# Performance work log

Measured on AMD Instinct MI355X. Metric: run time of the kernel, lower is better.

Reference implementation:

```python
import jax, jax.numpy as jnp
import numpy as np

# Problem dims
N_LIG, N_PROT = 10000, 40000
N = N_LIG + N_PROT            # total nodes in batched graph
E = 400000                    # total edges (avg degree 8)
B = 512                       # number of pocket graphs in batch
F_LIG, F_PROT = 74, 1280      # ligand / protein node feature dims
H, D = 4, 64                  # GAT heads, per-head dim
HD = H * D                    # hidden size == PROJ_DIM == 256


def setup_inputs() -> dict:
    key = jax.random.key(0)
    ks = jax.random.split(key, 16)
    s = jnp.float32(0.05)  # keep activations tame
    return {
        "ligand_x":  jax.random.normal(ks[0], (N_LIG, F_LIG), jnp.float32),
        "protein_x": jax.random.normal(ks[1], (N_PROT, F_PROT), jnp.float32),
        "W_lig":  jax.random.normal(ks[2], (F_LIG, HD), jnp.float32) * s,
        "W_prot": jax.random.normal(ks[3], (F_PROT, HD), jnp.float32) * s,
        "W1":     jax.random.normal(ks[4], (HD, HD), jnp.float32) * s,
        "a1_src": jax.random.normal(ks[5], (H, D), jnp.float32) * s,
        "a1_dst": jax.random.normal(ks[6], (H, D), jnp.float32) * s,
        "W2":     jax.random.normal(ks[7], (HD, HD), jnp.float32) * s,
        "a2_src": jax.random.normal(ks[8], (H, D), jnp.float32) * s,
        "a2_dst": jax.random.normal(ks[9], (H, D), jnp.float32) * s,
        "W_out":  jax.random.normal(ks[10], (HD + 1, 1), jnp.float32) * s,
        "b_out":  jnp.zeros((1,), jnp.float32),
        "edge_src":  jax.random.randint(ks[11], (E,), 0, N, jnp.int32),
        "edge_dst":  jax.random.randint(ks[12], (E,), 0, N, jnp.int32),
        "graph_ids": jnp.sort(jax.random.randint(ks[13], (N,), 0, B, jnp.int32)),
        "scores":    jax.random.uniform(ks[14], (B, 1), jnp.float32),
    }


def _gat_layer(x, W, a_src, a_dst, src, dst):
    """Multi-head GAT layer over an edge list. x:[N,HD] -> [N,HD]."""
    n = x.shape[0]
    h = (x @ W).reshape(n, H, D)                               # [N,H,D]
    att_s = jnp.einsum('nhd,hd->nh', h, a_src)                 # [N,H]
    att_d = jnp.einsum('nhd,hd->nh', h, a_dst)
    e = jax.nn.leaky_relu(att_s[src] + att_d[dst], 0.2)        # [E,H]
    # edge softmax over incoming edges of each destination node
    m = jax.ops.segment_max(e, dst, num_segments=n)            # [N,H]
    w = jnp.exp(e - m[dst])                                    # [E,H]
    denom = jax.ops.segment_sum(w, dst, num_segments=n)        # [N,H]
    agg = jax.ops.segment_sum(h[src] * w[..., None], dst, num_segments=n)  # [N,H,D]
    out = agg / (denom[..., None] + 1e-9)
    return jax.nn.elu(out).reshape(n, HD)


def reference(ligand_x, protein_x, W_lig, W_prot, W1, a1_src, a1_dst,
              W2, a2_src, a2_dst, W_out, b_out,
              edge_src, edge_dst, graph_ids, scores):
    # per-node-type input projection into shared hidden space
    x = jnp.concatenate([ligand_x @ W_lig, protein_x @ W_prot], axis=0)  # [N,HD]
    h = _gat_layer(x, W1, a1_src, a1_dst, edge_src, edge_dst)
    h = _gat_layer(h, W2, a2_src, a2_dst, edge_src, edge_dst)
    # mean pooling per graph -> [B, PROJ_DIM]
    gsum = jax.ops.segment_sum(h, graph_ids, num_segments=B)
    cnt = jax.ops.segment_sum(jnp.ones((h.shape[0], 1), h.dtype), graph_ids, num_segments=B)
    pooled = gsum / jnp.maximum(cnt, 1.0)
    # concat docking score, final linear (dropout is identity at eval)
    feat = jnp.concatenate([pooled, scores], axis=1)           # [B, PROJ_DIM+1]
    return feat @ W_out + b_out                                 # [B,1]
```

## Files before the change

kernel.cpp:

```cpp
#include <hip/hip_runtime.h>
#include <hip/hip_bf16.h>

#define N_LIG   10000
#define N_PROT  40000
#define NN      50000
#define EDGES   400000
#define BATCH   512
#define F_LIG   74
#define F_PROT  1280
#define HD      256
#define HEADS   4
#define DIM     64

typedef __bf16 bf16x8 __attribute__((ext_vector_type(8)));
typedef __bf16 bf16x4 __attribute__((ext_vector_type(4)));
typedef float  f32x4  __attribute__((ext_vector_type(4)));


__global__ void k_hist(const int* __restrict__ dst, int* __restrict__ counts, int E) {
    int e = blockIdx.x * blockDim.x + threadIdx.x;
    if (e < E) atomicAdd(&counts[dst[e]], 1);
}

__global__ __launch_bounds__(1024) void k_scan1(const int* __restrict__ counts,
                                                int* __restrict__ incl,
                                                int* __restrict__ bsum, int N) {
    __shared__ int tmp[1024];
    int i = blockIdx.x * 1024 + threadIdx.x;
    int v = (i < N) ? counts[i] : 0;
    tmp[threadIdx.x] = v;
    __syncthreads();
    for (int off = 1; off < 1024; off <<= 1) {
        int add = (threadIdx.x >= (unsigned)off) ? tmp[threadIdx.x - off] : 0;
        __syncthreads();
        tmp[threadIdx.x] += add;
        __syncthreads();
    }
    if (i < N) incl[i] = tmp[threadIdx.x];
    if (threadIdx.x == 1023) bsum[blockIdx.x] = tmp[1023];
}

__global__ void k_scan2(int* __restrict__ bsum, int nb, int* __restrict__ row_ptr, int N, int E) {
    if (threadIdx.x == 0 && blockIdx.x == 0) {
        int run = 0;
        for (int i = 0; i < nb; ++i) { int v = bsum[i]; bsum[i] = run; run += v; }
        row_ptr[N] = E;
    }
}

__global__ __launch_bounds__(1024) void k_scan3(const int* __restrict__ incl,
                                                const int* __restrict__ counts,
                                                const int* __restrict__ bsum,
                                                int* __restrict__ row_ptr, int N) {
    int i = blockIdx.x * 1024 + threadIdx.x;
    if (i < N) row_ptr[i] = bsum[blockIdx.x] + incl[i] - counts[i];
}

__global__ void k_scatter(const int* __restrict__ src, const int* __restrict__ dst,
                          const int* __restrict__ row_ptr, int* __restrict__ cursor,
                          int* __restrict__ csr_src, int E) {
    int e = blockIdx.x * blockDim.x + threadIdx.x;
    if (e < E) {
        int d = dst[e];
        int pos = row_ptr[d] + atomicAdd(&cursor[d], 1);
        csr_src[pos] = src[e];
    }
}

__global__ __launch_bounds__(256) void k_wcvt(const float* __restrict__ W,
                                              __bf16* __restrict__ Bt, int K, int Kp) {
    int n = blockIdx.x;
    for (int k = threadIdx.x; k < Kp; k += blockDim.x)
        Bt[(size_t)n * Kp + k] = (k < K) ? (__bf16)W[(size_t)k * HD + n] : (__bf16)0.f;
}

__global__ __launch_bounds__(128) void k_apad(const float* __restrict__ A, float* __restrict__ Ap) {
    int row = blockIdx.x, t = threadIdx.x;
    if (t < 96) Ap[(size_t)row * 96 + t] = (t < F_LIG) ? A[(size_t)row * F_LIG + t] : 0.f;
}

__device__ __forceinline__ void gload16(const void* g, void* l) {
    __builtin_amdgcn_global_load_lds(
        (const __attribute__((address_space(1))) void*)g,
        (__attribute__((address_space(3))) void*)l, 16, 0, 0);
}

__device__ __forceinline__ int xcd_swz(int orig, int nwg) {
    int q = nwg >> 3, r = nwg & 7;
    int xcd = orig & 7, idx = orig >> 3;
    return (xcd < r ? xcd * (q + 1) : r * (q + 1) + (xcd - r) * q) + idx;
}

template <int MODE>
__global__ __launch_bounds__(256, 3)
void mfma_gemm(const float* __restrict__ A, const __bf16* __restrict__ Bt,
               float* __restrict__ C,
               __bf16* __restrict__ Hbf, float* __restrict__ atts, float* __restrict__ attd,
               const float* __restrict__ a_src, const float* __restrict__ a_dst,
               int M, int K, int Kp, int nwg) {
    __shared__ __align__(16) unsigned char smem[49152];
    float*  sA = (float*)smem;
    __bf16* sB = (__bf16*)(smem + 24576);

    int wg   = xcd_swz(blockIdx.x, nwg);
    int tid  = threadIdx.x;
    int bm   = (wg >> 1) * 64;
    int bn   = (wg & 1) * 128;
    int lane = tid & 63, wave = tid >> 6;
    int wr   = wave >> 1, wc = wave & 1;
    int l15  = lane & 15, quad = lane >> 4;

    f32x4 acc[2][4];
    #pragma unroll
    for (int i = 0; i < 2; ++i)
        #pragma unroll
        for (int j = 0; j < 4; ++j)
            acc[i][j] = (f32x4){0.f, 0.f, 0.f, 0.f};

    int caA = wave * 2;
    int rlA = lane >> 3, csA = (lane & 7) ^ rlA;
    int rlB = lane >> 2, csB = (lane & 3) ^ (rlB & 3);

    int gmA[2];
    const __bf16* gB[2];
    #pragma unroll
    for (int it = 0; it < 2; ++it) {
        int gm = bm + (caA + it) * 8 + rlA;
        gmA[it] = (gm < M) ? gm : (M - 1);
        gB[it] = Bt + (size_t)(bn + (caA + it) * 16 + rlB) * Kp + csB * 8;
    }

    auto stage = [&](int buf, int k0) {
        #pragma unroll
        for (int it = 0; it < 2; ++it)
            gload16(A + (size_t)gmA[it] * K + k0 + csA * 4,
                    sA + buf * 2048 + (caA + it) * 256);
        #pragma unroll
        for (int it = 0; it < 2; ++it)
            gload16(gB[it] + k0,
                    sB + buf * 4096 + (caA + it) * 512);
    };

    int nsteps = K >> 5;

    stage(0, 0);
    if (nsteps > 1) {
        stage(1, 32);
        asm volatile("s_waitcnt vmcnt(4)" ::: "memory");
    } else {
        asm volatile("s_waitcnt vmcnt(0)" ::: "memory");
    }
    __builtin_amdgcn_s_barrier();
    __builtin_amdgcn_sched_barrier(0);

    int cur = 0, stg = 2;
    for (int s = 0; s < nsteps; ++s) {
        if (s + 2 < nsteps) stage(stg, (s + 2) * 32);

        bf16x8 bfr[4];
        #pragma unroll
        for (int j = 0; j < 4; ++j) {
            int rowb = wc * 64 + j * 16 + l15;
            int ch = quad ^ (l15 & 3);
            bfr[j] = *(const bf16x8*)&sB[cur * 4096 + rowb * 32 + ch * 8];
        }
        bf16x8 af[2], al[2];
        #pragma unroll
        for (int i = 0; i < 2; ++i) {
            int rowa = wr * 32 + i * 16 + l15;
            int ch0 = (quad * 2)     ^ (l15 & 7);
            int ch1 = (quad * 2 + 1) ^ (l15 & 7);
            f32x4 p0 = *(const f32x4*)&sA[cur * 2048 + rowa * 32 + ch0 * 4];
            f32x4 p1 = *(const f32x4*)&sA[cur * 2048 + rowa * 32 + ch1 * 4];
            #pragma unroll
            for (int c = 0; c < 8; ++c) {
                float x = (c < 4) ? p0[c] : p1[c - 4];
                __bf16 h = (__bf16)x;
                af[i][c] = h;
                if (MODE) al[i][c] = (__bf16)(x - (float)h);
            }
        }

        #pragma unroll
        for (int i = 0; i < 2; ++i)
            #pragma unroll
            for (int j = 0; j < 4; ++j) {
                acc[i][j] = __builtin_amdgcn_mfma_f32_16x16x32_bf16(af[i], bfr[j], acc[i][j], 0, 0, 0);
                if (MODE)
                    acc[i][j] = __builtin_amdgcn_mfma_f32_16x16x32_bf16(al[i], bfr[j], acc[i][j], 0, 0, 0);
            }

        asm volatile("s_waitcnt lgkmcnt(0)" ::: "memory");
        __builtin_amdgcn_sched_barrier(0);
        if (s + 2 < nsteps)      asm volatile("s_waitcnt vmcnt(4)" ::: "memory");
        else if (s + 1 < nsteps) asm volatile("s_waitcnt vmcnt(0)" ::: "memory");
        __builtin_amdgcn_s_barrier();
        __builtin_amdgcn_sched_barrier(0);

        cur = (cur == 2) ? 0 : cur + 1;
        stg = (stg == 2) ? 0 : stg + 1;
    }

    if (MODE == 0) {
        #pragma unroll
        for (int i = 0; i < 2; ++i)
            #pragma unroll
            for (int r = 0; r < 4; ++r) {
                int m = bm + wr * 32 + i * 16 + quad * 4 + r;
                if (m < M) {
                    #pragma unroll
                    for (int j = 0; j < 4; ++j)
                        C[(size_t)m * HD + bn + wc * 64 + j * 16 + l15] = acc[i][j][r];
                }
            }
    } else {
        int head = (bn >> 6) + wc;
        float as[4], ad2[4];
        #pragma unroll
        for (int j = 0; j < 4; ++j) {
            as[j]  = a_src[head * DIM + j * 16 + l15];
            ad2[j] = a_dst[head * DIM + j * 16 + l15];
        }
        #pragma unroll
        for (int i = 0; i < 2; ++i)
            #pragma unroll
            for (int r = 0; r < 4; ++r) {
                int m = bm + wr * 32 + i * 16 + quad * 4 + r;
                bool ok = m < M;
                float s = 0.f, t = 0.f;
                #pragma unroll
                for (int j = 0; j < 4; ++j) {
                    float v = acc[i][j][r];
                    if (ok) Hbf[(size_t)m * HD + head * DIM + j * 16 + l15] = (__bf16)v;
                    s += v * as[j];
                    t += v * ad2[j];
                }
                #pragma unroll
                for (int mask = 1; mask <= 8; mask <<= 1) {
                    s += __shfl_xor(s, mask, 64);
                    t += __shfl_xor(t, mask, 64);
                }
                if (ok && l15 == 0) {
                    atts[m * HEADS + head] = s;
                    attd[m * HEADS + head] = t;
                }
            }
    }
}

__global__ __launch_bounds__(256) void gat_agg(const __bf16* __restrict__ hW,
                                               const float* __restrict__ att_s,
                                               const float* __restrict__ att_d,
                                               const int* __restrict__ row_ptr,
                                               const int* __restrict__ csr_src,
                                               float* __restrict__ out, int N) {
    int n = blockIdx.x * 4 + (threadIdx.x >> 6);
    if (n >= N) return;
    int lane = threadIdx.x & 63;
    int sub  = lane >> 4;
    int dq   = lane & 15;
    int r0 = row_ptr[n], deg = row_ptr[n + 1] - r0;
    f32x4 ad4 = *(const f32x4*)&att_d[n * HEADS];

    f32x4 acc[4];
    #pragma unroll
    for (int h = 0; h < HEADS; ++h) acc[h] = (f32x4){0.f, 0.f, 0.f, 0.f};
    f32x4 wsum4 = (f32x4){0.f, 0.f, 0.f, 0.f};

    if (deg <= 64) {
        bool act = lane < deg;
        int sj = act ? csr_src[r0 + lane] : 0;
        f32x4 a4 = act ? *(const f32x4*)&att_s[sj * HEADS] : (f32x4){0.f, 0.f, 0.f, 0.f};
        f32x4 x4;
        #pragma unroll
        for (int h = 0; h < HEADS; ++h) {
            float v = a4[h] + ad4[h];
            v = (v >= 0.f) ? v : 0.2f * v;
            x4[h] = act ? v : -INFINITY;
        }
        f32x4 m4 = x4;
        for (int off = 32; off > 0; off >>= 1)
            #pragma unroll
            for (int h = 0; h < HEADS; ++h)
                m4[h] = fmaxf(m4[h], __shfl_xor(m4[h], off, 64));
        f32x4 w4;
        #pragma unroll
        for (int h = 0; h < HEADS; ++h)
            w4[h] = act ? expf(x4[h] - m4[h]) : 0.f;
        wsum4 = w4;

        for (int g0 = 0; g0 < deg; g0 += 4) {
            int e  = g0 + sub;
            int ec = min(e, deg - 1);
            int se = __shfl(sj, ec, 64);
            bool eact = e < deg;
            #pragma unroll
            for (int h = 0; h < HEADS; ++h) {
                float wh = __shfl(w4[h], ec, 64);
                if (!eact) wh = 0.f;
                bf16x4 v = *(const bf16x4*)&hW[(size_t)se * HD + h * DIM + dq * 4];
                #pragma unroll
                for (int c = 0; c < 4; ++c) acc[h][c] += wh * (float)v[c];
            }
        }
    } else {
        f32x4 m4 = (f32x4){-INFINITY, -INFINITY, -INFINITY, -INFINITY};
        for (int base = 0; base < deg; base += 64) {
            int i = base + lane;
            bool act = i < deg;
            int sj = act ? csr_src[r0 + i] : 0;
            f32x4 a4 = act ? *(const f32x4*)&att_s[sj * HEADS] : (f32x4){0.f, 0.f, 0.f, 0.f};
            #pragma unroll
            for (int h = 0; h < HEADS; ++h) {
                float v = a4[h] + ad4[h];
                v = (v >= 0.f) ? v : 0.2f * v;
                m4[h] = fmaxf(m4[h], act ? v : -INFINITY);
            }
        }
        for (int off = 32; off > 0; off >>= 1)
            #pragma unroll
            for (int h = 0; h < HEADS; ++h)
                m4[h] = fmaxf(m4[h], __shfl_xor(m4[h], off, 64));

        for (int base = 0; base < deg; base += 64) {
            int i = base + lane;
            bool act = i < deg;
            int sj = act ? csr_src[r0 + i] : 0;
            f32x4 a4 = act ? *(const f32x4*)&att_s[sj * HEADS] : (f32x4){0.f, 0.f, 0.f, 0.f};
            f32x4 w4;
            #pragma unroll
            for (int h = 0; h < HEADS; ++h) {
                float v = a4[h] + ad4[h];
                v = (v >= 0.f) ? v : 0.2f * v;
                w4[h] = act ? expf(v - m4[h]) : 0.f;
            }
            #pragma unroll
            for (int h = 0; h < HEADS; ++h) wsum4[h] += w4[h];
            int cnt = min(64, deg - base);
            for (int g0 = 0; g0 < cnt; g0 += 4) {
                int e  = g0 + sub;
                int ec = min(e, cnt - 1);
                int se = __shfl(sj, ec, 64);
                bool eact = e < cnt;
                #pragma unroll
                for (int h = 0; h < HEADS; ++h) {
                    float wh = __shfl(w4[h], ec, 64);
                    if (!eact) wh = 0.f;
                    bf16x4 v = *(const bf16x4*)&hW[(size_t)se * HD + h * DIM + dq * 4];
                    #pragma unroll
                    for (int c = 0; c < 4; ++c) acc[h][c] += wh * (float)v[c];
                }
            }
        }
    }

    #pragma unroll
    for (int h = 0; h < HEADS; ++h)
        #pragma unroll
        for (int c = 0; c < 4; ++c) {
            acc[h][c] += __shfl_xor(acc[h][c], 16, 64);
            acc[h][c] += __shfl_xor(acc[h][c], 32, 64);
        }
    for (int off = 32; off > 0; off >>= 1)
        #pragma unroll
        for (int h = 0; h < HEADS; ++h)
            wsum4[h] += __shfl_xor(wsum4[h], off, 64);

    if (sub == 0) {
        #pragma unroll
        for (int h = 0; h < HEADS; ++h) {
            float inv = 1.f / (wsum4[h] + 1e-9f);
            f32x4 o;
            #pragma unroll
            for (int c = 0; c < 4; ++c) {
                float v = acc[h][c] * inv;
                o[c] = (v > 0.f) ? v : expm1f(v);
            }
            *(f32x4*)&out[(size_t)n * HD + h * DIM + dq * 4] = o;
        }
    }
}

__global__ __launch_bounds__(256) void pool_out(const float* __restrict__ h,
                                                const int* __restrict__ gid,
                                                const float* __restrict__ W_out,
                                                const float* __restrict__ b_out,
                                                const float* __restrict__ scores,
                                                float* __restrict__ out, int N) {
    int b = blockIdx.x;
    int j = threadIdx.x;
    int l = 0, r = N;
    while (l < r) { int mid = (l + r) >> 1; if (gid[mid] < b) l = mid + 1; else r = mid; }
    int lo = l;
    r = N;
    while (l < r) { int mid = (l + r) >> 1; if (gid[mid] < b + 1) l = mid + 1; else r = mid; }
    int hi = l;

    float sum = 0.f;
    for (int n = lo; n < hi; ++n) sum += h[(size_t)n * HD + j];
    int cnt = hi - lo;
    float pooled = sum / fmaxf((float)cnt, 1.f);
    float val = pooled * W_out[j];

    __shared__ float red[256];
    red[j] = val;
    __syncthreads();
    for (int s = 128; s > 0; s >>= 1) {
        if (j < s) red[j] += red[j + s];
        __syncthreads();
    }
    if (j == 0) {
        out[b] = red[0] + scores[b] * W_out[HD] + b_out[0];
    }
}


static inline size_t al256(size_t x) { return (x + 255) & ~(size_t)255; }

#define KP_LIG  96
#define KP_PROT 1280
#define KP_HID  256

extern "C" void kernel_launch(void* const* d_in, const int* in_sizes, int n_in,
                              void* d_out, int out_size, void* d_ws, size_t ws_size,
                              hipStream_t stream) {
    const float* ligand_x  = (const float*)d_in[0];
    const float* protein_x = (const float*)d_in[1];
    const float* W_lig     = (const float*)d_in[2];
    const float* W_prot    = (const float*)d_in[3];
    const float* W1        = (const float*)d_in[4];
    const float* a1_src    = (const float*)d_in[5];
    const float* a1_dst    = (const float*)d_in[6];
    const float* W2        = (const float*)d_in[7];
    const float* a2_src    = (const float*)d_in[8];
    const float* a2_dst    = (const float*)d_in[9];
    const float* W_out     = (const float*)d_in[10];
    const float* b_out     = (const float*)d_in[11];
    const int*   edge_src  = (const int*)d_in[12];
    const int*   edge_dst  = (const int*)d_in[13];
    const int*   graph_ids = (const int*)d_in[14];
    const float* scores    = (const float*)d_in[15];
    float* out = (float*)d_out;

    char* w = (char*)d_ws;
    float*  xbuf = (float*)w;           w += al256((size_t)NN * HD * 4);
    __bf16* Hbf  = (__bf16*)w;          w += al256((size_t)NN * HD * 2);
    float* atts = (float*)w;            w += al256((size_t)NN * HEADS * 4);
    float* attd = (float*)w;            w += al256((size_t)NN * HEADS * 4);
    int* counts  = (int*)w;             w += al256((size_t)NN * 4);
    int* incl    = (int*)w;             w += al256((size_t)NN * 4);
    int* bsum    = (int*)w;             w += al256(64 * 4);
    int* row_ptr = (int*)w;             w += al256((size_t)(NN + 1) * 4);
    int* cursor  = (int*)w;             w += al256((size_t)NN * 4);
    int* csr_src = (int*)w;             w += al256((size_t)EDGES * 4);
    __bf16* Bt_lig  = (__bf16*)w;       w += al256((size_t)HD * KP_LIG * 2);
    __bf16* Bt_prot = (__bf16*)w;       w += al256((size_t)HD * KP_PROT * 2);
    __bf16* Bt_W1   = (__bf16*)w;       w += al256((size_t)HD * KP_HID * 2);
    __bf16* Bt_W2   = (__bf16*)w;       w += al256((size_t)HD * KP_HID * 2);
    float* Apad     = (float*)w;        w += al256((size_t)N_LIG * KP_LIG * 4);

    const int NB_SCAN = (NN + 1023) / 1024;

    hipMemsetAsync(counts, 0, (size_t)NN * 4, stream);
    hipMemsetAsync(cursor, 0, (size_t)NN * 4, stream);

    k_wcvt<<<HD, 256, 0, stream>>>(W_lig,  Bt_lig,  F_LIG,  KP_LIG);
    k_wcvt<<<HD, 256, 0, stream>>>(W_prot, Bt_prot, F_PROT, KP_PROT);
    k_wcvt<<<HD, 256, 0, stream>>>(W1,     Bt_W1,   HD,     KP_HID);
    k_wcvt<<<HD, 256, 0, stream>>>(W2,     Bt_W2,   HD,     KP_HID);
    k_apad<<<N_LIG, 128, 0, stream>>>(ligand_x, Apad);

    k_hist<<<(EDGES + 255) / 256, 256, 0, stream>>>(edge_dst, counts, EDGES);
    k_scan1<<<NB_SCAN, 1024, 0, stream>>>(counts, incl, bsum, NN);
    k_scan2<<<1, 1, 0, stream>>>(bsum, NB_SCAN, row_ptr, NN, EDGES);
    k_scan3<<<NB_SCAN, 1024, 0, stream>>>(incl, counts, bsum, row_ptr, NN);
    k_scatter<<<(EDGES + 255) / 256, 256, 0, stream>>>(edge_src, edge_dst, row_ptr,
                                                       cursor, csr_src, EDGES);

    {
        int nwg = 2 * ((N_LIG + 63) / 64);
        mfma_gemm<0><<<nwg, 256, 0, stream>>>(
            Apad, Bt_lig, xbuf, nullptr, nullptr, nullptr, nullptr, nullptr,
            N_LIG, KP_LIG, KP_LIG, nwg);
    }
    {
        int nwg = 2 * ((N_PROT + 63) / 64);
        mfma_gemm<0><<<nwg, 256, 0, stream>>>(
            protein_x, Bt_prot, xbuf + (size_t)N_LIG * HD, nullptr, nullptr, nullptr,
            nullptr, nullptr, N_PROT, KP_PROT, KP_PROT, nwg);
    }

    {
        int nwg = 2 * ((NN + 63) / 64);
        mfma_gemm<1><<<nwg, 256, 0, stream>>>(
            xbuf, Bt_W1, nullptr, Hbf, atts, attd, a1_src, a1_dst, NN, KP_HID, KP_HID, nwg);
    }
    gat_agg<<<(NN + 3) / 4, 256, 0, stream>>>(Hbf, atts, attd, row_ptr, csr_src, xbuf, NN);

    {
        int nwg = 2 * ((NN + 63) / 64);
        mfma_gemm<1><<<nwg, 256, 0, stream>>>(
            xbuf, Bt_W2, nullptr, Hbf, atts, attd, a2_src, a2_dst, NN, KP_HID, KP_HID, nwg);
    }
    gat_agg<<<(NN + 3) / 4, 256, 0, stream>>>(Hbf, atts, attd, row_ptr, csr_src, xbuf, NN);

    pool_out<<<BATCH, 256, 0, stream>>>(xbuf, graph_ids, W_out, b_out, scores, out, NN);
}
```

Before: 668.7 us.

## Widen GEMM tile to full 256 columns so each A tile is loaded once

Changes the MFMA GEMM block tile from 64x128 to 64x256 so one workgroup covers the whole hidden dimension. Each wave now owns one 64-column head slice, and the 64-row A tile is read from global once instead of by two workgroups. The B staging buffer doubles, LDS grows to 72KB, per-wave accumulators double, and occupancy is lowered from 3 to 2 blocks per CU. The trade-off is higher register and LDS pressure plus half as many workgroups against halved A traffic and fp32-to-bf16 conversion work.

```diff
diff --git a/kernel.cpp b/kernel.cpp
--- a/kernel.cpp
+++ b/kernel.cpp
@@ -92,53 +92,52 @@
 }
 
 template <int MODE>
-__global__ __launch_bounds__(256, 3)
+__global__ __launch_bounds__(256, 2)
 void mfma_gemm(const float* __restrict__ A, const __bf16* __restrict__ Bt,
                float* __restrict__ C,
                __bf16* __restrict__ Hbf, float* __restrict__ atts, float* __restrict__ attd,
                const float* __restrict__ a_src, const float* __restrict__ a_dst,
                int M, int K, int Kp, int nwg) {
-    __shared__ __align__(16) unsigned char smem[49152];
+    __shared__ __align__(16) unsigned char smem[73728];
     float*  sA = (float*)smem;
     __bf16* sB = (__bf16*)(smem + 24576);
 
     int wg   = xcd_swz(blockIdx.x, nwg);
     int tid  = threadIdx.x;
-    int bm   = (wg >> 1) * 64;
-    int bn   = (wg & 1) * 128;
+    int bm   = wg * 64;
     int lane = tid & 63, wave = tid >> 6;
-    int wr   = wave >> 1, wc = wave & 1;
     int l15  = lane & 15, quad = lane >> 4;
 
-    f32x4 acc[2][4];
+    f32x4 acc[4][4];
     #pragma unroll
-    for (int i = 0; i < 2; ++i)
+    for (int i = 0; i < 4; ++i)
         #pragma unroll
         for (int j = 0; j < 4; ++j)
             acc[i][j] = (f32x4){0.f, 0.f, 0.f, 0.f};
 
-    int caA = wave * 2;
     int rlA = lane >> 3, csA = (lane & 7) ^ rlA;
     int rlB = lane >> 2, csB = (lane & 3) ^ (rlB & 3);
 
     int gmA[2];
-    const __bf16* gB[2];
+    const __bf16* gB[4];
     #pragma unroll
     for (int it = 0; it < 2; ++it) {
-        int gm = bm + (caA + it) * 8 + rlA;
+        int gm = bm + (wave * 2 + it) * 8 + rlA;
         gmA[it] = (gm < M) ? gm : (M - 1);
-        gB[it] = Bt + (size_t)(bn + (caA + it) * 16 + rlB) * Kp + csB * 8;
-    }
+    }
+    #pragma unroll
+    for (int it = 0; it < 4; ++it)
+        gB[it] = Bt + (size_t)((wave * 4 + it) * 16 + rlB) * Kp + csB * 8;
 
     auto stage = [&](int buf, int k0) {
         #pragma unroll
         for (int it = 0; it < 2; ++it)
             gload16(A + (size_t)gmA[it] * K + k0 + csA * 4,
-                    sA + buf * 2048 + (caA + it) * 256);
-        #pragma unroll
-        for (int it = 0; it < 2; ++it)
+                    sA + buf * 2048 + (wave * 2 + it) * 256);
+        #pragma unroll
+        for (int it = 0; it < 4; ++it)
             gload16(gB[it] + k0,
-                    sB + buf * 4096 + (caA + it) * 512);
+                    sB + buf * 8192 + (wave * 4 + it) * 512);
     };
 
     int nsteps = K >> 5;
@@ -146,7 +145,7 @@
     stage(0, 0);
     if (nsteps > 1) {
         stage(1, 32);
-        asm volatile("s_waitcnt vmcnt(4)" ::: "memory");
+        asm volatile("s_waitcnt vmcnt(6)" ::: "memory");
     } else {
         asm volatile("s_waitcnt vmcnt(0)" ::: "memory");
     }
@@ -160,14 +159,14 @@
         bf16x8 bfr[4];
         #pragma unroll
         for (int j = 0; j < 4; ++j) {
-            int rowb = wc * 64 + j * 16 + l15;
+            int rowb = wave * 64 + j * 16 + l15;
             int ch = quad ^ (l15 & 3);
-            bfr[j] = *(const bf16x8*)&sB[cur * 4096 + rowb * 32 + ch * 8];
-        }
-        bf16x8 af[2], al[2];
-        #pragma unroll
-        for (int i = 0; i < 2; ++i) {
-            int rowa = wr * 32 + i * 16 + l15;
+            bfr[j] = *(const bf16x8*)&sB[cur * 8192 + rowb * 32 + ch * 8];
+        }
+        bf16x8 af[4], al[4];
+        #pragma unroll
+        for (int i = 0; i < 4; ++i) {
+            int rowa = i * 16 + l15;
             int ch0 = (quad * 2)     ^ (l15 & 7);
             int ch1 = (quad * 2 + 1) ^ (l15 & 7);
             f32x4 p0 = *(const f32x4*)&sA[cur * 2048 + rowa * 32 + ch0 * 4];
@@ -182,7 +181,7 @@
         }
 
         #pragma unroll
-        for (int i = 0; i < 2; ++i)
+        for (int i = 0; i < 4; ++i)
             #pragma unroll
             for (int j = 0; j < 4; ++j) {
                 acc[i][j] = __builtin_amdgcn_mfma_f32_16x16x32_bf16(af[i], bfr[j], acc[i][j], 0, 0, 0);
@@ -192,8 +191,8 @@
 
         asm volatile("s_waitcnt lgkmcnt(0)" ::: "memory");
         __builtin_amdgcn_sched_barrier(0);
-        if (s + 2 < nsteps)      asm volatile("s_waitcnt vmcnt(4)" ::: "memory");
-        else if (s + 1 < nsteps) asm volatile("s_waitcnt vmcnt(0)" ::: "memory");
+        if (s + 2 < nsteps)      { asm volatile("s_waitcnt vmcnt(6)" ::: "memory"); }
+        else if (s + 1 < nsteps) { asm volatile("s_waitcnt vmcnt(0)" ::: "memory"); }
         __builtin_amdgcn_s_barrier();
         __builtin_amdgcn_sched_barrier(0);
 
@@ -203,18 +202,18 @@
 
     if (MODE == 0) {
         #pragma unroll
-        for (int i = 0; i < 2; ++i)
+        for (int i = 0; i < 4; ++i)
             #pragma unroll
             for (int r = 0; r < 4; ++r) {
-                int m = bm + wr * 32 + i * 16 + quad * 4 + r;
+                int m = bm + i * 16 + quad * 4 + r;
                 if (m < M) {
                     #pragma unroll
                     for (int j = 0; j < 4; ++j)
-                        C[(size_t)m * HD + bn + wc * 64 + j * 16 + l15] = acc[i][j][r];
+                        C[(size_t)m * HD + wave * 64 + j * 16 + l15] = acc[i][j][r];
                 }
             }
     } else {
-        int head = (bn >> 6) + wc;
+        int head = wave;
         float as[4], ad2[4];
         #pragma unroll
         for (int j = 0; j < 4; ++j) {
@@ -222,10 +221,10 @@
             ad2[j] = a_dst[head * DIM + j * 16 + l15];
         }
         #pragma unroll
-        for (int i = 0; i < 2; ++i)
+        for (int i = 0; i < 4; ++i)
             #pragma unroll
             for (int r = 0; r < 4; ++r) {
-                int m = bm + wr * 32 + i * 16 + quad * 4 + r;
+                int m = bm + i * 16 + quad * 4 + r;
                 bool ok = m < M;
                 float s = 0.f, t = 0.f;
                 #pragma unroll
@@ -478,27 +477,27 @@
                                                        cursor, csr_src, EDGES);
 
     {
-        int nwg = 2 * ((N_LIG + 63) / 64);
+        int nwg = (N_LIG + 63) / 64;
         mfma_gemm<0><<<nwg, 256, 0, stream>>>(
             Apad, Bt_lig, xbuf, nullptr, nullptr, nullptr, nullptr, nullptr,
             N_LIG, KP_LIG, KP_LIG, nwg);
     }
     {
-        int nwg = 2 * ((N_PROT + 63) / 64);
+        int nwg = (N_PROT + 63) / 64;
         mfma_gemm<0><<<nwg, 256, 0, stream>>>(
             protein_x, Bt_prot, xbuf + (size_t)N_LIG * HD, nullptr, nullptr, nullptr,
             nullptr, nullptr, N_PROT, KP_PROT, KP_PROT, nwg);
     }
 
     {
-        int nwg = 2 * ((NN + 63) / 64);
+        int nwg = (NN + 63) / 64;
         mfma_gemm<1><<<nwg, 256, 0, stream>>>(
             xbuf, Bt_W1, nullptr, Hbf, atts, attd, a1_src, a1_dst, NN, KP_HID, KP_HID, nwg);
     }
     gat_agg<<<(NN + 3) / 4, 256, 0, stream>>>(Hbf, atts, attd, row_ptr, csr_src, xbuf, NN);
 
     {
-        int nwg = 2 * ((NN + 63) / 64);
+        int nwg = (NN + 63) / 64;
         mfma_gemm<1><<<nwg, 256, 0, stream>>>(
             xbuf, Bt_W2, nullptr, Hbf, atts, attd, a2_src, a2_dst, NN, KP_HID, KP_HID, nwg);
     }
```

After: 660.2 us. About the same (-1.3%).
